# Performance work log

Hardware: AMD Instinct MI355X
Metric: run time of the kernel (lower is better)

Reference implementation:

```python
import jax, jax.numpy as jnp
import numpy as np
from jax import lax

S = 20      # max_segments
D = 1000    # traj_dict entries
L = 200     # dmp_traj_length
CONV_OUT = 512 * 4 * 4  # 8192 for 100x100 input


def _conv(x, w, b):
    # NCHW valid conv, kernel 3x3, stride 1 (matches nn.Conv2d defaults)
    y = lax.conv_general_dilated(x, w, (1, 1), 'VALID',
                                 dimension_numbers=('NCHW', 'OIHW', 'NCHW'))
    return y + b[None, :, None, None]


def _pool2(x):
    # max_pool2d(kernel=2, stride=2), floor mode == VALID reduce_window
    return lax.reduce_window(x, -jnp.inf, lax.max, (1, 1, 2, 2), (1, 1, 2, 2), 'VALID')


def setup_inputs() -> dict:
    key = jax.random.key(0)
    ks = jax.random.split(key, 20)
    f32 = jnp.float32

    def rn(k, shape, s):
        return jax.random.normal(k, shape, dtype=f32) * s

    x = jax.random.normal(ks[0], (128, 3, 100, 100), dtype=f32)
    w1 = rn(ks[1], (64, 3, 3, 3), 0.1);    b1 = jnp.zeros((64,), f32)
    w2 = rn(ks[2], (128, 64, 3, 3), 0.04); b2 = jnp.zeros((128,), f32)
    w3 = rn(ks[3], (256, 128, 3, 3), 0.03); b3 = jnp.zeros((256,), f32)
    w4 = rn(ks[4], (512, 256, 3, 3), 0.02); b4 = jnp.zeros((512,), f32)
    out_size = 2 + 3 * S
    fw1 = rn(ks[5], (CONV_OUT, 2048), 0.01); fb1 = jnp.zeros((2048,), f32)
    fw2 = rn(ks[6], (2048, 2048), 0.02);     fb2 = jnp.zeros((2048,), f32)
    fw3 = rn(ks[7], (2048, out_size), 0.02); fb3 = jnp.zeros((out_size,), f32)
    traj_dict = jax.random.normal(ks[8], (D, L, 2), dtype=f32)
    return {
        'x': x,
        'w1': w1, 'b1': b1, 'w2': w2, 'b2': b2,
        'w3': w3, 'b3': b3, 'w4': w4, 'b4': b4,
        'fw1': fw1, 'fb1': fb1, 'fw2': fw2, 'fb2': fb2,
        'fw3': fw3, 'fb3': fb3,
        'traj_dict': traj_dict,
    }


def _forward(x, w1, b1, w2, b2, w3, b3, w4, b4,
             fw1, fb1, fw2, fb2, fw3, fb3, traj_dict):
    # conv encoder (relu(maxpool(conv)) x4, matching the torch order)
    h = jax.nn.relu(_pool2(_conv(x, w1, b1)))
    h = jax.nn.relu(_pool2(_conv(h, w2, b2)))
    h = jax.nn.relu(_pool2(_conv(h, w3, b3)))
    h = jax.nn.relu(_pool2(_conv(h, w4, b4)))
    h = h.reshape(h.shape[0], -1)                      # [B, 8192]
    # FC stack: tanh on hidden layers, linear head (dropout p=0 / eval)
    h = jnp.tanh(h @ fw1 + fb1)
    h = jnp.tanh(h @ fw2 + fb2)
    p = h @ fw3 + fb3                                  # [B, 2 + 3S]

    B = p.shape[0]
    init_pos = p[:, :2]                                # [B, 2]
    seg = p[:, 2:].reshape(B, S, 3)                    # (dict_idx, x_scale, y_scale)

    # getTrajFromDict: the loop of round/clamp/sign/abs one-hot masks is exactly
    # a gather at the clamped rounded index (round is half-to-even in both torch and jax)
    idx = jnp.clip(jnp.round(seg[..., 0]), 0, D - 1).astype(jnp.int32)  # [B, S]
    base = traj_dict[idx]                              # [B, S, L, 2]

    scaled = base * seg[:, :, None, 1:3]               # [B, S, L, 2]
    # chain segments: each segment starts at previous segment's endpoint
    offsets = scaled[:, :, -1, :]                      # [B, S, 2]
    starts = init_pos[:, None, :] + jnp.cumsum(offsets, axis=1) - offsets  # exclusive cumsum
    traj = (scaled + starts[:, :, None, :]).reshape(B, S * L, 2)
    return traj


def reference(x, w1, b1, w2, b2, w3, b3, w4, b4,
              fw1, fb1, fw2, fb2, fw3, fb3, traj_dict):
    return _forward(x, w1, b1, w2, b2, w3, b3, w4, b4,
                    fw1, fb1, fw2, fb2, fw3, fb3, traj_dict)
```

## Files before the change

kernel.cpp:

```cpp
#include <hip/hip_runtime.h>
#include <hip/hip_bf16.h>

typedef __attribute__((ext_vector_type(8))) short s8v;
typedef __attribute__((ext_vector_type(4))) float f4v;
typedef unsigned short ushort;
typedef unsigned int uint;

union V8 { s8v v; short s[8]; };

__device__ __forceinline__ short f2bf(float v){
    union { __hip_bfloat16 b; short u; } x;
    x.b = __float2bfloat16(v);
    return x.u;
}
__device__ __forceinline__ float bf2f(short u){
    union { short u; __hip_bfloat16 b; } x;
    x.u = u;
    return __bfloat162float(x.b);
}
__device__ __forceinline__ void splitf(float v, short& h, short& l){
    h = f2bf(v);
    l = f2bf(v - bf2f(h));
}
__device__ __forceinline__ uint packsplit(float v){
    short h, l; splitf(v, h, l);
    return (uint)(ushort)h | ((uint)(ushort)l << 16);
}

template<int CIN, int HIN, int PH, int OCB, int SPT, int CICH, int COUT>
__global__ __launch_bounds__(SPT) void k_conv_pool_relu(
    const float* __restrict__ in, const float* __restrict__ w,
    const float* __restrict__ bias, uint* __restrict__ out)
{
    constexpr int WIN   = HIN;
    constexpr int PW    = PH;
    constexpr int WSTR  = CICH * 9 + 1;

    __shared__ float wsh[OCB * WSTR];

    const int b   = blockIdx.z;
    const int oc0 = blockIdx.y * OCB;
    const int t   = threadIdx.x;
    const int sp  = blockIdx.x * SPT + t;
    const bool active = sp < PH * PW;
    const int py = active ? (sp / PW) : 0;
    const int px = active ? (sp % PW) : 0;

    float acc[OCB][4];
#pragma unroll
    for (int j = 0; j < OCB; ++j)
        acc[j][0] = acc[j][1] = acc[j][2] = acc[j][3] = 0.f;

    const float* inb = in + (size_t)b * CIN * HIN * WIN;

    for (int c0 = 0; c0 < CIN; c0 += CICH) {
        __syncthreads();
        for (int i = t; i < OCB * CICH * 9; i += SPT) {
            int j = i / (CICH * 9);
            int r = i - j * (CICH * 9);
            wsh[j * WSTR + r] = w[((size_t)(oc0 + j) * CIN + c0) * 9 + r];
        }
        __syncthreads();

        for (int ci = 0; ci < CICH; ++ci) {
            const float* inc = inb + (size_t)(c0 + ci) * HIN * WIN
                             + (2 * py) * WIN + 2 * px;
            float patch[4][4];
#pragma unroll
            for (int r = 0; r < 4; ++r)
#pragma unroll
                for (int c = 0; c < 4; ++c)
                    patch[r][c] = inc[r * WIN + c];

#pragma unroll
            for (int j = 0; j < OCB; ++j) {
                const float* wp = &wsh[j * WSTR + ci * 9];
#pragma unroll
                for (int kh = 0; kh < 3; ++kh)
#pragma unroll
                    for (int kw = 0; kw < 3; ++kw) {
                        float wv = wp[kh * 3 + kw];
                        acc[j][0] = fmaf(patch[kh][kw],         wv, acc[j][0]);
                        acc[j][1] = fmaf(patch[kh][kw + 1],     wv, acc[j][1]);
                        acc[j][2] = fmaf(patch[kh + 1][kw],     wv, acc[j][2]);
                        acc[j][3] = fmaf(patch[kh + 1][kw + 1], wv, acc[j][3]);
                    }
            }
        }
    }

    if (active) {
        uint tmp[OCB];
#pragma unroll
        for (int j = 0; j < OCB; ++j) {
            float m = fmaxf(fmaxf(acc[j][0], acc[j][1]),
                            fmaxf(acc[j][2], acc[j][3]));
            m = fmaxf(m + bias[oc0 + j], 0.f);
            tmp[j] = packsplit(m);
        }
        uint* ob = out + ((size_t)b * PH * PW + sp) * COUT + oc0;
#pragma unroll
        for (int q = 0; q < OCB / 4; ++q)
            ((uint4*)ob)[q] = ((const uint4*)tmp)[q];
    }
}

__global__ void k_wsplit_perm(const float* __restrict__ w, ushort* __restrict__ oh,
                              ushort* __restrict__ ol, int CIN, int total)
{
    int i = blockIdx.x * 256 + threadIdx.x;
    if (i < total) {
        int K = CIN * 9;
        int n = i / K;
        int rem = i - n * K;
        int ci = rem / 9;
        int r = rem - 9 * ci;
        short h, l; splitf(w[i], h, l);
        size_t o = (size_t)n * K + r * CIN + ci;
        oh[o] = (ushort)h; ol[o] = (ushort)l;
    }
}

__global__ __launch_bounds__(256) void k_wsplitT(
    const float* __restrict__ B, ushort* __restrict__ oh, ushort* __restrict__ ol,
    int K, int N)
{
    __shared__ float tl[32][33];
    const int n0 = blockIdx.x * 32, k0 = blockIdx.y * 32;
    const int r = threadIdx.x >> 5, c = threadIdx.x & 31;
#pragma unroll
    for (int it = 0; it < 4; ++it) {
        int row = r + it * 8;
        tl[row][c] = B[(size_t)(k0 + row) * N + n0 + c];
    }
    __syncthreads();
#pragma unroll
    for (int it = 0; it < 4; ++it) {
        int a = r + it * 8;
        float v = tl[c][a];
        short h, l; splitf(v, h, l);
        size_t o = (size_t)(n0 + a) * K + k0 + c;
        oh[o] = (ushort)h; ol[o] = (ushort)l;
    }
}

template<int MODE, int BPRE, int EPI, int LOG2CIN, int K, int KCH, int N,
         int HIN, int PPH, int PPW, int COUT, int TPI>
__global__ __launch_bounds__(256) void k_gemm4(
    const void* __restrict__ A0, const void* __restrict__ A1,
    const void* __restrict__ B0, const void* __restrict__ B1,
    const float* __restrict__ bias, void* __restrict__ O0, void* __restrict__ O1)
{
    constexpr int CIN = 1 << LOG2CIN;
    constexpr int HH  = HIN * HIN;

    __shared__ short Ah[64][40], Al[64][40], Bh[128][40], Bl[128][40];

    const int t    = threadIdx.x;
    const int lane = t & 63;
    const int wave = t >> 6;
    const int n0   = blockIdx.y * 128;
    const int sArow = t & 63, sAoct = t >> 6;
    const int sBrow = t & 127, sBo = t >> 7;

    const uint*   ArI = nullptr;
    const ushort* Ahg = nullptr;
    const ushort* Alg = nullptr;
    int b = 0, ptile = 0, kbeg = 0, kend = K;

    if (MODE == 0) {
        b = blockIdx.x / TPI;
        ptile = blockIdx.x - b * TPI;
        int pl = ptile * 16 + (sArow >> 2);
        int quad = sArow & 3;
        int py = 0, px = 0;
        if (pl < PPH * PPW) { py = pl / PPW; px = pl - py * PPW; }
        ArI = (const uint*)A0
            + ((size_t)b * HH + (size_t)(2 * py + (quad >> 1)) * HIN
               + (2 * px + (quad & 1))) * CIN;
    } else {
        int arow = blockIdx.x * 64 + sArow;
        Ahg = (const ushort*)A0 + (size_t)arow * K;
        Alg = (const ushort*)A1 + (size_t)arow * K;
        kbeg = blockIdx.z * KCH;
        kend = kbeg + KCH;
    }

    auto pfA = [&](int kkx, V8& ha, V8& la) {
        const int kb = kkx + sAoct * 8;
        if (MODE == 0) {
            const int r  = kb >> LOG2CIN;
            const int cb = kb & (CIN - 1);
            const int rh = (r * 11) >> 5;
            const int rw = r - 3 * rh;
            const uint* g = ArI + (rh * HIN + rw) * CIN + cb;
            uint4 v0 = *(const uint4*)g;
            uint4 v1 = *(const uint4*)(g + 4);
            uint vv[8] = {v0.x, v0.y, v0.z, v0.w, v1.x, v1.y, v1.z, v1.w};
#pragma unroll
            for (int j = 0; j < 8; ++j) {
                ha.s[j] = (short)(vv[j] & 0xffffu);
                la.s[j] = (short)(vv[j] >> 16);
            }
        } else {
            ha.v = *(const s8v*)(Ahg + kb);
            la.v = *(const s8v*)(Alg + kb);
        }
    };
    auto pfB = [&](int kkx, V8* hb, V8* lb) {
#pragma unroll
        for (int q = 0; q < 2; ++q) {
            const int o = sBo + 2 * q;
            const int kb = kkx + o * 8;
            if (BPRE) {
                hb[q].v = *(const s8v*)((const ushort*)B0 + (size_t)(n0 + sBrow) * K + kb);
                lb[q].v = *(const s8v*)((const ushort*)B1 + (size_t)(n0 + sBrow) * K + kb);
            } else if (MODE == 0) {
                const int r  = kb >> LOG2CIN;
                const int cb = kb & (CIN - 1);
                const float* bp = (const float*)B0
                    + (size_t)(n0 + sBrow) * K + (size_t)cb * 9 + r;
#pragma unroll
                for (int j = 0; j < 8; ++j)
                    splitf(bp[9 * j], hb[q].s[j], lb[q].s[j]);
            } else {
                const float* bp = (const float*)B0 + (size_t)kb * N + n0 + sBrow;
#pragma unroll
                for (int j = 0; j < 8; ++j)
                    splitf(bp[(size_t)j * N], hb[q].s[j], lb[q].s[j]);
            }
        }
    };

    f4v acc[2][4];
    const f4v z4 = {0.f, 0.f, 0.f, 0.f};
#pragma unroll
    for (int i = 0; i < 2; ++i)
#pragma unroll
        for (int j = 0; j < 4; ++j) acc[i][j] = z4;

    V8 pAh, pAl, pBh[2], pBl[2];
    pfA(kbeg, pAh, pAl);
    pfB(kbeg, pBh, pBl);

    for (int kk = kbeg; kk < kend; kk += 32) {
        __syncthreads();
        *(s8v*)&Ah[sArow][sAoct * 8] = pAh.v;
        *(s8v*)&Al[sArow][sAoct * 8] = pAl.v;
#pragma unroll
        for (int q = 0; q < 2; ++q) {
            const int o = sBo + 2 * q;
            *(s8v*)&Bh[sBrow][o * 8] = pBh[q].v;
            *(s8v*)&Bl[sBrow][o * 8] = pBl[q].v;
        }
        if (kk + 32 < kend) {
            pfA(kk + 32, pAh, pAl);
            pfB(kk + 32, pBh, pBl);
        }
        __syncthreads();

        const int fm = lane & 15;
        const int fk = (lane >> 4) * 8;
        s8v a_h[2], a_l[2], b_h[4], b_l[4];
#pragma unroll
        for (int i = 0; i < 2; ++i) {
            a_h[i] = *(const s8v*)&Ah[(wave & 1) * 32 + i * 16 + fm][fk];
            a_l[i] = *(const s8v*)&Al[(wave & 1) * 32 + i * 16 + fm][fk];
        }
#pragma unroll
        for (int j = 0; j < 4; ++j) {
            b_h[j] = *(const s8v*)&Bh[(wave >> 1) * 64 + j * 16 + fm][fk];
            b_l[j] = *(const s8v*)&Bl[(wave >> 1) * 64 + j * 16 + fm][fk];
        }
#define MF(a_, b_, c_) c_ = __builtin_amdgcn_mfma_f32_16x16x32_bf16(a_, b_, c_, 0, 0, 0)
#pragma unroll
        for (int i = 0; i < 2; ++i)
#pragma unroll
            for (int j = 0; j < 4; ++j) {
                MF(a_h[i], b_h[j], acc[i][j]);
                MF(a_h[i], b_l[j], acc[i][j]);
                MF(a_l[i], b_h[j], acc[i][j]);
            }
#undef MF
    }

    if (MODE == 0) {
        const int PP = PPH * PPW;
#pragma unroll
        for (int i = 0; i < 2; ++i)
#pragma unroll
            for (int j = 0; j < 4; ++j) {
                int p  = ptile * 16 + (wave & 1) * 8 + i * 4 + (lane >> 4);
                int oc = n0 + (wave >> 1) * 64 + j * 16 + (lane & 15);
                if (p < PP) {
                    f4v v = acc[i][j];
                    float m = fmaxf(fmaxf(v.x, v.y), fmaxf(v.z, v.w));
                    m = fmaxf(m + bias[oc], 0.f);
                    if (EPI == 0) {
                        ((uint*)O0)[((size_t)b * PP + p) * COUT + oc] = packsplit(m);
                    } else {
                        size_t o = (size_t)(b * COUT + oc) * PP + p;
                        short h, l; splitf(m, h, l);
                        ((ushort*)O0)[o] = (ushort)h;
                        ((ushort*)O1)[o] = (ushort)l;
                    }
                }
            }
    } else {
        float* P = (float*)O0 + (size_t)blockIdx.z * 128 * N;
#pragma unroll
        for (int i = 0; i < 2; ++i)
#pragma unroll
            for (int j = 0; j < 4; ++j) {
                int n = n0 + (wave >> 1) * 64 + j * 16 + (lane & 15);
                int mb = blockIdx.x * 64 + (wave & 1) * 32 + i * 16 + (lane >> 4) * 4;
                f4v v = acc[i][j];
                P[(size_t)(mb + 0) * N + n] = v.x;
                P[(size_t)(mb + 1) * N + n] = v.y;
                P[(size_t)(mb + 2) * N + n] = v.z;
                P[(size_t)(mb + 3) * N + n] = v.w;
            }
    }
}

template<int EFMT>
__global__ void k_fc_epi2(const float* __restrict__ P, const float* __restrict__ bias,
                          ushort* __restrict__ oh, ushort* __restrict__ ol,
                          float* __restrict__ of, int MN, int N, int KS)
{
    int i = blockIdx.x * 256 + threadIdx.x;
    if (i >= MN) return;
    float s = 0.f;
    for (int z = 0; z < KS; ++z) s += P[(size_t)z * MN + i];
    s = tanhf(s + bias[i % N]);
    if (EFMT == 1) {
        short h, l; splitf(s, h, l);
        oh[i] = (ushort)h; ol[i] = (ushort)l;
    } else {
        of[i] = s;
    }
}

__global__ __launch_bounds__(64) void k_fc3_part(
    const float* __restrict__ A, const float* __restrict__ B,
    float* __restrict__ P, int K, int N, int KS)
{
    const int m = blockIdx.x, kz = blockIdx.y;
    const int n = threadIdx.x;
    const int kchunk = K / KS;
    if (n < N) {
        float acc = 0.f;
        const float* Am = A + (size_t)m * K;
        const int ke = (kz + 1) * kchunk;
        for (int k = kz * kchunk; k < ke; ++k)
            acc = fmaf(Am[k], B[(size_t)k * N + n], acc);
        P[((size_t)kz * 128 + m) * N + n] = acc;
    }
}

__global__ void k_fc_epi(const float* __restrict__ P, const float* __restrict__ bias,
                         float* __restrict__ out, int MN, int N, int KS)
{
    int i = blockIdx.x * 256 + threadIdx.x;
    if (i >= MN) return;
    float s = 0.f;
    for (int z = 0; z < KS; ++z) s += P[(size_t)z * MN + i];
    out[i] = s + bias[i % N];
}

__global__ void k_traj_start(const float* __restrict__ p, const float* __restrict__ td,
                             float* __restrict__ starts, float* __restrict__ sa,
                             int* __restrict__ sidx)
{
    int b = threadIdx.x;
    const float* pb = p + b * 62;
    float cx = pb[0], cy = pb[1];
    for (int s = 0; s < 20; ++s) {
        float f  = pb[2 + 3 * s];
        float a0 = pb[3 + 3 * s];
        float a1 = pb[4 + 3 * s];
        int idx = (int)fminf(fmaxf(rintf(f), 0.f), 999.f);
        int bs = b * 20 + s;
        sidx[bs] = idx;
        sa[bs * 2 + 0] = a0;
        sa[bs * 2 + 1] = a1;
        starts[bs * 2 + 0] = cx;
        starts[bs * 2 + 1] = cy;
        cx += td[((size_t)idx * 200 + 199) * 2 + 0] * a0;
        cy += td[((size_t)idx * 200 + 199) * 2 + 1] * a1;
    }
}

__global__ void k_traj_main(const float* __restrict__ td, const float* __restrict__ starts,
                            const float* __restrict__ sa, const int* __restrict__ sidx,
                            float* __restrict__ out)
{
    int bs = blockIdx.x;
    int idx = sidx[bs];
    float a0 = sa[bs * 2 + 0], a1 = sa[bs * 2 + 1];
    float s0 = starts[bs * 2 + 0], s1 = starts[bs * 2 + 1];
    const float* row = td + (size_t)idx * 400;
    float* o = out + (size_t)bs * 400;
    for (int e = threadIdx.x; e < 400; e += blockDim.x) {
        float v = row[e];
        o[e] = (e & 1) ? fmaf(v, a1, s1) : fmaf(v, a0, s0);
    }
}

template<int BPRE>
static void run_all(void* const* d_in, float* out, char* ws, hipStream_t stream)
{
    const float* x   = (const float*)d_in[0];
    const float* w1  = (const float*)d_in[1];
    const float* b1  = (const float*)d_in[2];
    const float* w2  = (const float*)d_in[3];
    const float* b2  = (const float*)d_in[4];
    const float* w3  = (const float*)d_in[5];
    const float* b3  = (const float*)d_in[6];
    const float* w4  = (const float*)d_in[7];
    const float* b4  = (const float*)d_in[8];
    const float* fw1 = (const float*)d_in[9];
    const float* fb1 = (const float*)d_in[10];
    const float* fw2 = (const float*)d_in[11];
    const float* fb2 = (const float*)d_in[12];
    const float* fw3 = (const float*)d_in[13];
    const float* fb3 = (const float*)d_in[14];
    const float* td  = (const float*)d_in[15];

    uint*   h1   = (uint*)ws;
    uint*   h2   = (uint*)(ws + 78675968ull);
    uint*   h3   = (uint*)ws;
    ushort* fw1h = (ushort*)(ws + 13107200ull);
    ushort* fw1l = (ushort*)(ws + 46661632ull);
    ushort* h4h  = (ushort*)(ws + 80216064ull);
    ushort* h4l  = (ushort*)(ws + 82313216ull);
    ushort* fw2h = (ushort*)(ws + 84410368ull);
    ushort* fw2l = (ushort*)(ws + 92798976ull);
    float*  part = (float*)(ws + 101187584ull);
    ushort* a1h  = (ushort*)(ws + 109576192ull);
    ushort* a1l  = (ushort*)(ws + 110100480ull);
    float*  a2   = (float*)(ws + 110624768ull);
    float*  p    = (float*)(ws + 111673344ull);
    float*  starts = (float*)(ws + 111705088ull);
    float*  sa   = (float*)(ws + 111725568ull);
    int*    sidx = (int*)(ws + 111746048ull);
    ushort* w2h = (ushort*)(ws + 113344512ull);
    ushort* w2l = (ushort*)(ws + 113491968ull);
    ushort* w3h = (ushort*)(ws + 113639424ull);
    ushort* w3l = (ushort*)(ws + 114229248ull);
    ushort* w4h = (ushort*)(ws + 114819072ull);
    ushort* w4l = (ushort*)(ws + 117178368ull);

    if (BPRE) {
        k_wsplit_perm<<<(73728 + 255) / 256, 256, 0, stream>>>(w2, w2h, w2l, 64, 73728);
        k_wsplit_perm<<<(294912 + 255) / 256, 256, 0, stream>>>(w3, w3h, w3l, 128, 294912);
        k_wsplit_perm<<<(1179648 + 255) / 256, 256, 0, stream>>>(w4, w4h, w4l, 256, 1179648);
    }

    k_conv_pool_relu<3, 100, 49, 16, 256, 3, 64>
        <<<dim3(10, 4, 128), 256, 0, stream>>>(x, w1, b1, h1);

    k_gemm4<0, BPRE, 0, 6, 576, 576, 128, 49, 23, 23, 128, 34>
        <<<dim3(34 * 128, 1), 256, 0, stream>>>(
            h1, nullptr, BPRE ? (const void*)w2h : (const void*)w2,
            BPRE ? (const void*)w2l : nullptr, b2, h2, nullptr);
    k_gemm4<0, BPRE, 0, 7, 1152, 1152, 256, 23, 10, 10, 256, 7>
        <<<dim3(7 * 128, 2), 256, 0, stream>>>(
            h2, nullptr, BPRE ? (const void*)w3h : (const void*)w3,
            BPRE ? (const void*)w3l : nullptr, b3, h3, nullptr);

    if (BPRE) {
        k_wsplitT<<<dim3(2048 / 32, 8192 / 32), 256, 0, stream>>>(fw1, fw1h, fw1l, 8192, 2048);
        k_wsplitT<<<dim3(2048 / 32, 2048 / 32), 256, 0, stream>>>(fw2, fw2h, fw2l, 2048, 2048);
    }

    k_gemm4<0, BPRE, 1, 8, 2304, 2304, 512, 10, 4, 4, 512, 1>
        <<<dim3(128, 4), 256, 0, stream>>>(
            h3, nullptr, BPRE ? (const void*)w4h : (const void*)w4,
            BPRE ? (const void*)w4l : nullptr, b4, h4h, h4l);

    k_gemm4<1, BPRE, 2, 0, 8192, 1024, 2048, 1, 1, 1, 1, 1>
        <<<dim3(2, 16, 8), 256, 0, stream>>>(
            h4h, h4l, BPRE ? (const void*)fw1h : (const void*)fw1,
            BPRE ? (const void*)fw1l : nullptr, nullptr, part, nullptr);
    k_fc_epi2<1><<<(128 * 2048 + 255) / 256, 256, 0, stream>>>(
        part, fb1, a1h, a1l, nullptr, 128 * 2048, 2048, 8);
    k_gemm4<1, BPRE, 2, 0, 2048, 256, 2048, 1, 1, 1, 1, 1>
        <<<dim3(2, 16, 8), 256, 0, stream>>>(
            a1h, a1l, BPRE ? (const void*)fw2h : (const void*)fw2,
            BPRE ? (const void*)fw2l : nullptr, nullptr, part, nullptr);
    k_fc_epi2<2><<<(128 * 2048 + 255) / 256, 256, 0, stream>>>(
        part, fb2, nullptr, nullptr, a2, 128 * 2048, 2048, 8);

    k_fc3_part<<<dim3(128, 4), 64, 0, stream>>>(a2, fw3, part, 2048, 62, 4);
    k_fc_epi<<<(128 * 62 + 255) / 256, 256, 0, stream>>>(
        part, fb3, p, 128 * 62, 62, 4);
    k_traj_start<<<1, 128, 0, stream>>>(p, td, starts, sa, sidx);
    k_traj_main<<<2560, 256, 0, stream>>>(td, starts, sa, sidx, out);
}

extern "C" void kernel_launch(void* const* d_in, const int* in_sizes, int n_in,
                              void* d_out, int out_size, void* d_ws, size_t ws_size,
                              hipStream_t stream)
{
    (void)in_sizes; (void)n_in; (void)out_size;
    if (ws_size >= 119537664ull)
        run_all<1>(d_in, (float*)d_out, (char*)d_ws, stream);
    else
        run_all<0>(d_in, (float*)d_out, (char*)d_ws, stream);
}
```

Measured before the change: 1.045 ms.

## Double-buffer LDS tiles in split-bf16 GEMM and use octet-major layout

The GEMM kernel now keeps two shared-memory buffers for the A/B hi/lo tiles. The next tile is stored into the alternate buffer after the MFMA block, so each k-step needs one barrier instead of two. The LDS layout also changes from padded row-major [row][40] to octet-major contiguous 8-element vectors, aiming for conflict-free 16-byte reads. The trade is twice the LDS footprint, which may reduce occupancy, and prefetched registers stay live across the MFMA section.

```diff
diff --git a/kernel.cpp b/kernel.cpp
--- a/kernel.cpp
+++ b/kernel.cpp
@@ -146,7 +146,7 @@
 
 template<int MODE, int BPRE, int EPI, int LOG2CIN, int K, int KCH, int N,
          int HIN, int PPH, int PPW, int COUT, int TPI>
-__global__ __launch_bounds__(256) void k_gemm4(
+__global__ __launch_bounds__(256) void k_gemm5(
     const void* __restrict__ A0, const void* __restrict__ A1,
     const void* __restrict__ B0, const void* __restrict__ B1,
     const float* __restrict__ bias, void* __restrict__ O0, void* __restrict__ O1)
@@ -154,7 +154,8 @@
     constexpr int CIN = 1 << LOG2CIN;
     constexpr int HH  = HIN * HIN;
 
-    __shared__ short Ah[64][40], Al[64][40], Bh[128][40], Bl[128][40];
+    __shared__ short As[2][2][4 * 64 * 8];
+    __shared__ short Bs[2][2][4 * 128 * 8];
 
     const int t    = threadIdx.x;
     const int lane = t & 63;
@@ -231,6 +232,16 @@
             }
         }
     };
+    auto stAB = [&](int buf, const V8& ha, const V8& la, const V8* hb, const V8* lb) {
+        *(s8v*)&As[buf][0][(sAoct * 64 + sArow) * 8] = ha.v;
+        *(s8v*)&As[buf][1][(sAoct * 64 + sArow) * 8] = la.v;
+#pragma unroll
+        for (int q = 0; q < 2; ++q) {
+            const int o = sBo + 2 * q;
+            *(s8v*)&Bs[buf][0][(o * 128 + sBrow) * 8] = hb[q].v;
+            *(s8v*)&Bs[buf][1][(o * 128 + sBrow) * 8] = lb[q].v;
+        }
+    };
 
     f4v acc[2][4];
     const f4v z4 = {0.f, 0.f, 0.f, 0.f};
@@ -242,35 +253,32 @@
     V8 pAh, pAl, pBh[2], pBl[2];
     pfA(kbeg, pAh, pAl);
     pfB(kbeg, pBh, pBl);
-
+    stAB(0, pAh, pAl, pBh, pBl);
+
+    const int fm  = lane & 15;
+    const int fo  = lane >> 4;
+    const int amr = (wave & 1) * 32 + fm;
+    const int bnr = (wave >> 1) * 64 + fm;
+
+    int buf = 0;
     for (int kk = kbeg; kk < kend; kk += 32) {
         __syncthreads();
-        *(s8v*)&Ah[sArow][sAoct * 8] = pAh.v;
-        *(s8v*)&Al[sArow][sAoct * 8] = pAl.v;
-#pragma unroll
-        for (int q = 0; q < 2; ++q) {
-            const int o = sBo + 2 * q;
-            *(s8v*)&Bh[sBrow][o * 8] = pBh[q].v;
-            *(s8v*)&Bl[sBrow][o * 8] = pBl[q].v;
-        }
-        if (kk + 32 < kend) {
+        const bool more = (kk + 32 < kend);
+        if (more) {
             pfA(kk + 32, pAh, pAl);
             pfB(kk + 32, pBh, pBl);
         }
-        __syncthreads();
-
-        const int fm = lane & 15;
-        const int fk = (lane >> 4) * 8;
+
         s8v a_h[2], a_l[2], b_h[4], b_l[4];
 #pragma unroll
         for (int i = 0; i < 2; ++i) {
-            a_h[i] = *(const s8v*)&Ah[(wave & 1) * 32 + i * 16 + fm][fk];
-            a_l[i] = *(const s8v*)&Al[(wave & 1) * 32 + i * 16 + fm][fk];
+            a_h[i] = *(const s8v*)&As[buf][0][(fo * 64 + amr + i * 16) * 8];
+            a_l[i] = *(const s8v*)&As[buf][1][(fo * 64 + amr + i * 16) * 8];
         }
 #pragma unroll
         for (int j = 0; j < 4; ++j) {
-            b_h[j] = *(const s8v*)&Bh[(wave >> 1) * 64 + j * 16 + fm][fk];
-            b_l[j] = *(const s8v*)&Bl[(wave >> 1) * 64 + j * 16 + fm][fk];
+            b_h[j] = *(const s8v*)&Bs[buf][0][(fo * 128 + bnr + j * 16) * 8];
+            b_l[j] = *(const s8v*)&Bs[buf][1][(fo * 128 + bnr + j * 16) * 8];
         }
 #define MF(a_, b_, c_) c_ = __builtin_amdgcn_mfma_f32_16x16x32_bf16(a_, b_, c_, 0, 0, 0)
 #pragma unroll
@@ -282,6 +290,9 @@
                 MF(a_l[i], b_h[j], acc[i][j]);
             }
 #undef MF
+        if (more)
+            stAB(buf ^ 1, pAh, pAl, pBh, pBl);
+        buf ^= 1;
     }
 
     if (MODE == 0) {
@@ -460,11 +471,11 @@
     k_conv_pool_relu<3, 100, 49, 16, 256, 3, 64>
         <<<dim3(10, 4, 128), 256, 0, stream>>>(x, w1, b1, h1);
 
-    k_gemm4<0, BPRE, 0, 6, 576, 576, 128, 49, 23, 23, 128, 34>
+    k_gemm5<0, BPRE, 0, 6, 576, 576, 128, 49, 23, 23, 128, 34>
         <<<dim3(34 * 128, 1), 256, 0, stream>>>(
             h1, nullptr, BPRE ? (const void*)w2h : (const void*)w2,
             BPRE ? (const void*)w2l : nullptr, b2, h2, nullptr);
-    k_gemm4<0, BPRE, 0, 7, 1152, 1152, 256, 23, 10, 10, 256, 7>
+    k_gemm5<0, BPRE, 0, 7, 1152, 1152, 256, 23, 10, 10, 256, 7>
         <<<dim3(7 * 128, 2), 256, 0, stream>>>(
             h2, nullptr, BPRE ? (const void*)w3h : (const void*)w3,
             BPRE ? (const void*)w3l : nullptr, b3, h3, nullptr);
@@ -474,18 +485,18 @@
         k_wsplitT<<<dim3(2048 / 32, 2048 / 32), 256, 0, stream>>>(fw2, fw2h, fw2l, 2048, 2048);
     }
 
-    k_gemm4<0, BPRE, 1, 8, 2304, 2304, 512, 10, 4, 4, 512, 1>
+    k_gemm5<0, BPRE, 1, 8, 2304, 2304, 512, 10, 4, 4, 512, 1>
         <<<dim3(128, 4), 256, 0, stream>>>(
             h3, nullptr, BPRE ? (const void*)w4h : (const void*)w4,
             BPRE ? (const void*)w4l : nullptr, b4, h4h, h4l);
 
-    k_gemm4<1, BPRE, 2, 0, 8192, 1024, 2048, 1, 1, 1, 1, 1>
+    k_gemm5<1, BPRE, 2, 0, 8192, 1024, 2048, 1, 1, 1, 1, 1>
         <<<dim3(2, 16, 8), 256, 0, stream>>>(
             h4h, h4l, BPRE ? (const void*)fw1h : (const void*)fw1,
             BPRE ? (const void*)fw1l : nullptr, nullptr, part, nullptr);
     k_fc_epi2<1><<<(128 * 2048 + 255) / 256, 256, 0, stream>>>(
         part, fb1, a1h, a1l, nullptr, 128 * 2048, 2048, 8);
-    k_gemm4<1, BPRE, 2, 0, 2048, 256, 2048, 1, 1, 1, 1, 1>
+    k_gemm5<1, BPRE, 2, 0, 2048, 256, 2048, 1, 1, 1, 1, 1>
         <<<dim3(2, 16, 8), 256, 0, stream>>>(
             a1h, a1l, BPRE ? (const void*)fw2h : (const void*)fw2,
             BPRE ? (const void*)fw2l : nullptr, nullptr, part, nullptr);
```

Measured after the change: 1.047 ms. No clear change (+0.2%).
